# Kernel optimization log

Measured on AMD Instinct MI355X. Metric: run time of the kernel, lower is better.

The kernel has to match this reference:

```python
import jax, jax.numpy as jnp
import numpy as np

N = 100000      # nodes
E = 1250000     # edges
F_IN = 32       # node_feat_dim
H = 64          # hidden_dim (hard-coded in module)
R = 8           # num_relations
G = 256         # graphs in batch
EMB = 16        # embedding_dim
OUT = 1         # output_dim
EPS = 1e-5


def setup_inputs() -> dict:
    key = jax.random.key(0)
    ks = jax.random.split(key, 40)
    w = lambda k, shape: (jax.random.normal(k, shape, jnp.float32) * 0.05)
    inp = {
        'x': jax.random.normal(ks[0], (N, F_IN), jnp.float32),
        'edge_index': jax.random.randint(ks[1], (2, E), 0, N),
        'edge_type': jax.random.randint(ks[2], (E,), 0, R),
        'batch': jnp.sort(jax.random.randint(ks[3], (N,), 0, G)),
        # RGCN layer params: per-relation weight, root weight, bias
        'conv1_w': w(ks[4], (R, F_IN, H)), 'conv1_root': w(ks[5], (F_IN, H)), 'conv1_b': jnp.zeros((H,), jnp.float32),
        'bn1_g': jnp.ones((H,), jnp.float32), 'bn1_b': jnp.zeros((H,), jnp.float32),
        'conv2_w': w(ks[6], (R, H, H)), 'conv2_root': w(ks[7], (H, H)), 'conv2_b': jnp.zeros((H,), jnp.float32),
        'bn2_g': jnp.ones((H,), jnp.float32), 'bn2_b': jnp.zeros((H,), jnp.float32),
        'conv3_w': w(ks[8], (R, H, H)), 'conv3_root': w(ks[9], (H, H)), 'conv3_b': jnp.zeros((H,), jnp.float32),
        'bn3_g': jnp.ones((H,), jnp.float32), 'bn3_b': jnp.zeros((H,), jnp.float32),
        # fc_emb: Linear(384->128), BN(128), LeakyReLU, Dropout(eval=id), Linear(128->EMB)
        'fc1_w': w(ks[10], (3 * H * 2, 128)), 'fc1_b': jnp.zeros((128,), jnp.float32),
        'fcbn_g': jnp.ones((128,), jnp.float32), 'fcbn_b': jnp.zeros((128,), jnp.float32),
        'fc2_w': w(ks[11], (128, EMB)), 'fc2_b': jnp.zeros((EMB,), jnp.float32),
        # decoder: Linear(EMB->64), LeakyReLU, Linear(64->OUT)
        'dec1_w': w(ks[12], (EMB, 64)), 'dec1_b': jnp.zeros((64,), jnp.float32),
        'dec2_w': w(ks[13], (64, OUT)), 'dec2_b': jnp.zeros((OUT,), jnp.float32),
    }
    return inp


def _leaky(z):
    return jnp.where(z > 0, z, 0.2 * z)


def _bn(x, g, b):  # training-mode batch norm, biased variance
    mu = x.mean(axis=0)
    var = x.var(axis=0)
    return g * (x - mu) * jax.lax.rsqrt(var + EPS) + b


def _rgcn(x, W, root, bias, src, dst, edge_type):
    # out_i = x_i @ root + bias + sum_r mean_{j in N_r(i)} x_j @ W_r
    out = x @ root + bias
    for r in range(R):
        mask = (edge_type == r).astype(x.dtype)           # [E]
        h = x @ W[r]                                      # [N, out]
        msg = h[src] * mask[:, None]                      # gather + mask
        s = jax.ops.segment_sum(msg, dst, num_segments=N)  # scatter-add
        cnt = jax.ops.segment_sum(mask, dst, num_segments=N)
        out = out + s / jnp.maximum(cnt, 1.0)[:, None]
    return out


def reference(x, edge_index, edge_type, batch,
              conv1_w, conv1_root, conv1_b, bn1_g, bn1_b,
              conv2_w, conv2_root, conv2_b, bn2_g, bn2_b,
              conv3_w, conv3_root, conv3_b, bn3_g, bn3_b,
              fc1_w, fc1_b, fcbn_g, fcbn_b, fc2_w, fc2_b,
              dec1_w, dec1_b, dec2_w, dec2_b):
    src, dst = edge_index[0], edge_index[1]
    x1 = jax.nn.relu(_bn(_rgcn(x, conv1_w, conv1_root, conv1_b, src, dst, edge_type), bn1_g, bn1_b))
    x2 = jax.nn.relu(_bn(_rgcn(x1, conv2_w, conv2_root, conv2_b, src, dst, edge_type), bn2_g, bn2_b))
    x3 = jax.nn.relu(_bn(_rgcn(x2, conv3_w, conv3_root, conv3_b, src, dst, edge_type), bn3_g, bn3_b))
    x_all = jnp.concatenate([x1, x2, x3], axis=1)         # [N, 3H]
    ones = jnp.ones((N,), x.dtype)
    cnt = jax.ops.segment_sum(ones, batch, num_segments=G)
    pool_mean = jax.ops.segment_sum(x_all, batch, num_segments=G) / jnp.maximum(cnt, 1.0)[:, None]
    pool_max = jax.ops.segment_max(x_all, batch, num_segments=G)
    pool_max = jnp.where(jnp.isfinite(pool_max), pool_max, 0.0)
    x_graph = jnp.concatenate([pool_mean, pool_max], axis=1)  # [G, 6H]
    h = _leaky(_bn(x_graph @ fc1_w + fc1_b, fcbn_g, fcbn_b))  # dropout = identity (eval)
    emb = h @ fc2_w + fc2_b                                   # [G, EMB]
    pred = _leaky(emb @ dec1_w + dec1_b) @ dec2_w + dec2_b    # [G, OUT]
    return (pred, emb)
```

## Files before the change

kernel.cpp:

```cpp
#include <hip/hip_runtime.h>

#define NN 100000
#define NE 1250000
#define FIN 32
#define HD 64
#define NR 8
#define NG 256
#define BN_EPS 1e-5f
#define PCH 100
#define M_KEYS (NN * NR)
#define NB 782
#define RREP 32
#define HW 576

#if defined(__has_builtin)
#if __has_builtin(__builtin_amdgcn_fdot2_f32_bf16)
#define USE_DOT2 1
#endif
#endif
#ifndef USE_DOT2
#define USE_DOT2 0
#endif

typedef unsigned short ushort_t;
typedef __attribute__((ext_vector_type(8))) short short8;
typedef __attribute__((ext_vector_type(4))) float f32x4;
typedef __attribute__((ext_vector_type(4))) unsigned int u32x4;
#if USE_DOT2
typedef __bf16 bf16x2 __attribute__((ext_vector_type(2)));
#endif

static __device__ __forceinline__ ushort_t f2bf(float f) {
  unsigned u = __float_as_uint(f);
  u += 0x7fffu + ((u >> 16) & 1u);
  return (ushort_t)(u >> 16);
}
static __device__ __forceinline__ float bf2f(ushort_t b) {
  return __uint_as_float((unsigned)b << 16);
}

__global__ void k_zero(float* __restrict__ p, int n) {
  int i = blockIdx.x * 256 + threadIdx.x;
  if (i < n) p[i] = 0.0f;
}

__global__ void k_cnt(const int* __restrict__ dst, const int* __restrict__ ty,
                      unsigned* __restrict__ cnt, int* __restrict__ rank) {
  int e = blockIdx.x * 256 + threadIdx.x;
  if (e < NE) {
    int key = dst[e] * NR + ty[e];
    rank[e] = (int)atomicAdd(&cnt[key], 1u);
  }
}

__global__ void k_scanA(const unsigned* __restrict__ cnt, unsigned* __restrict__ bsum) {
  __shared__ unsigned red[256];
  int t = threadIdx.x;
  int base = blockIdx.x * 1024 + t * 4;
  unsigned s = 0;
  #pragma unroll
  for (int i = 0; i < 4; i++) {
    int idx = base + i;
    if (idx < M_KEYS) s += cnt[idx];
  }
  red[t] = s;
  __syncthreads();
  for (int off = 128; off > 0; off >>= 1) {
    if (t < off) red[t] += red[t + off];
    __syncthreads();
  }
  if (t == 0) bsum[blockIdx.x] = red[0];
}

__global__ __launch_bounds__(1024) void k_scanB(const unsigned* __restrict__ bsum,
                                                unsigned* __restrict__ boff,
                                                int* __restrict__ rowstart) {
  __shared__ unsigned sb[1024];
  int t = threadIdx.x;
  unsigned mine = (t < NB) ? bsum[t] : 0u;
  sb[t] = mine;
  __syncthreads();
  for (int off = 1; off < 1024; off <<= 1) {
    unsigned v = (t >= off) ? sb[t - off] : 0u;
    __syncthreads();
    sb[t] += v;
    __syncthreads();
  }
  if (t < NB) boff[t] = sb[t] - mine;
  if (t == 1023) rowstart[M_KEYS] = (int)sb[1023];
}

__global__ void k_scanC(const unsigned* __restrict__ cnt, const unsigned* __restrict__ boff,
                        int* __restrict__ rowstart) {
  __shared__ unsigned sb[256];
  int t = threadIdx.x;
  int base = blockIdx.x * 1024 + t * 4;
  unsigned c0 = (base + 0 < M_KEYS) ? cnt[base + 0] : 0u;
  unsigned c1 = (base + 1 < M_KEYS) ? cnt[base + 1] : 0u;
  unsigned c2 = (base + 2 < M_KEYS) ? cnt[base + 2] : 0u;
  unsigned c3 = (base + 3 < M_KEYS) ? cnt[base + 3] : 0u;
  unsigned tot = c0 + c1 + c2 + c3;
  sb[t] = tot;
  __syncthreads();
  for (int off = 1; off < 256; off <<= 1) {
    unsigned v = (t >= off) ? sb[t - off] : 0u;
    __syncthreads();
    sb[t] += v;
    __syncthreads();
  }
  unsigned run = boff[blockIdx.x] + (sb[t] - tot);
  if (base + 0 < M_KEYS) rowstart[base + 0] = (int)run; run += c0;
  if (base + 1 < M_KEYS) rowstart[base + 1] = (int)run; run += c1;
  if (base + 2 < M_KEYS) rowstart[base + 2] = (int)run; run += c2;
  if (base + 3 < M_KEYS) rowstart[base + 3] = (int)run;
}

__global__ void k_place(const int* __restrict__ src, const int* __restrict__ dst,
                        const int* __restrict__ ty, const int* __restrict__ rank,
                        const int* __restrict__ rowstart, unsigned* __restrict__ eb) {
  int e = blockIdx.x * 256 + threadIdx.x;
  if (e < NE) {
    int t = ty[e];
    int key = dst[e] * NR + t;
    unsigned off = (unsigned)(src[e] * HW + t * 64);
    eb[rowstart[key] + rank[e]] = (off << 3) | (unsigned)t;
  }
}

template <int F>
__global__ void k_wconv(const float* __restrict__ convw, const float* __restrict__ root,
                        ushort_t* __restrict__ wt) {
  int i = blockIdx.x * 256 + threadIdx.x;
  if (i >= 576 * F) return;
  int c = i / F, k = i % F;
  float v = (c < 512) ? convw[((size_t)(c >> 6) * F + k) * 64 + (c & 63)]
                      : root[(size_t)k * 64 + (c & 63)];
  wt[(size_t)c * F + k] = f2bf(v);
}

template <int F, bool APPLY_BN>
__global__ __launch_bounds__(256) void k_xmm(
    const float* __restrict__ xin, const float* __restrict__ scsh,
    const ushort_t* __restrict__ wt, ushort_t* __restrict__ h) {
  constexpr int KK = 2 * F;
  constexpr int XPAD = KK + 8;
  constexpr int LDR = 592;
  __shared__ ushort_t xs[16 * XPAD];
  __shared__ ushort_t ot[16 * LDR];
  int lane = threadIdx.x & 63;
  int w = threadIdx.x >> 6;
  int m = lane & 15;
  int q = lane >> 4;
  int ct0 = w * 9;

  short8 bfrag[9 * (F / 32)];
  #pragma unroll
  for (int ks = 0; ks < F / 32; ks++)
    #pragma unroll
    for (int t = 0; t < 9; t++)
      bfrag[ks * 9 + t] =
          *(const short8*)(wt + (size_t)((ct0 + t) * 16 + m) * F + ks * 32 + q * 8);

  for (int tile = blockIdx.x; tile < NN / 16; tile += gridDim.x) {
    int nbase = tile * 16;
    for (int i = threadIdx.x; i < 16 * F; i += 256) {
      int r = i / F, k = i - r * F;
      float v = xin[(size_t)(nbase + r) * F + k];
      if (APPLY_BN) v = fmaxf(fmaf(v, scsh[k], scsh[64 + k]), 0.0f);
      ushort_t hi = f2bf(v);
      xs[r * XPAD + k] = hi;
      xs[r * XPAD + F + k] = f2bf(v - bf2f(hi));
    }
    __syncthreads();

    short8 afrag[2 * (F / 32)];
    #pragma unroll
    for (int ks = 0; ks < F / 32; ks++) {
      afrag[2 * ks + 0] = *(const short8*)&xs[m * XPAD + ks * 32 + q * 8];
      afrag[2 * ks + 1] = *(const short8*)&xs[m * XPAD + F + ks * 32 + q * 8];
    }

    f32x4 acc[9];
    #pragma unroll
    for (int t = 0; t < 9; t++) acc[t] = (f32x4){0.f, 0.f, 0.f, 0.f};
    #pragma unroll
    for (int ks = 0; ks < F / 32; ks++) {
      #pragma unroll
      for (int t = 0; t < 9; t++) {
        acc[t] = __builtin_amdgcn_mfma_f32_16x16x32_bf16(afrag[2 * ks + 0],
                                                         bfrag[ks * 9 + t], acc[t], 0, 0, 0);
        acc[t] = __builtin_amdgcn_mfma_f32_16x16x32_bf16(afrag[2 * ks + 1],
                                                         bfrag[ks * 9 + t], acc[t], 0, 0, 0);
      }
    }
    #pragma unroll
    for (int t = 0; t < 9; t++) {
      int col = (ct0 + t) * 16 + m;
      #pragma unroll
      for (int j = 0; j < 4; j++) {
        int row = q * 4 + j;
        ot[row * LDR + col] = f2bf(acc[t][j]);
      }
    }
    __syncthreads();
    u32x4* dst = (u32x4*)(h + (size_t)nbase * HW);
    for (int idx = threadIdx.x; idx < 16 * 72; idx += 256) {
      int row = idx / 72, i = idx - row * 72;
      dst[row * 72 + i] = *(const u32x4*)&ot[row * LDR + i * 8];
    }
  }
}

__global__ __launch_bounds__(256) void k_agg4(
    const ushort_t* __restrict__ h, const int* __restrict__ rs,
    const unsigned* __restrict__ eb, const float* __restrict__ bias,
    float* __restrict__ outp, float* __restrict__ statsrep) {
  __shared__ float red[512];
  __shared__ ushort_t iclu[4][8];
  int lane = threadIdx.x & 63, w = threadIdx.x >> 6;
  int n = blockIdx.x * 4 + w;
  if (lane < 8) {
    int c = rs[n * NR + lane + 1] - rs[n * NR + lane];
    iclu[w][lane] = f2bf(1.0f / (float)(c > 1 ? c : 1));
  }
  int lo = rs[n * NR];
  int cnt = rs[n * NR + NR] - lo;
  __syncthreads();
  int g = lane >> 4;
  int c4 = (lane & 15) * 4;
  float a0 = 0.f, a1 = 0.f, a2 = 0.f, a3 = 0.f;
  for (int base = 0; base < cnt; base += 32) {
    unsigned rec[8]; uint2 hv[8]; unsigned icb[8];
    #pragma unroll
    for (int s = 0; s < 8; s++) {
      int el = base + s * 4 + g;
      rec[s] = eb[lo + (el < cnt ? el : cnt - 1)];
      icb[s] = (el < cnt) ? (unsigned)iclu[w][rec[s] & 7] : 0u;
    }
    #pragma unroll
    for (int s = 0; s < 8; s++)
      hv[s] = *(const uint2*)(h + (size_t)(rec[s] >> 3) + c4);
#if USE_DOT2
    #pragma unroll
    for (int s = 0; s < 8; s += 2) {
      unsigned b01 = __builtin_amdgcn_perm(icb[s + 1], icb[s], 0x05040100u);
      unsigned p0 = __builtin_amdgcn_perm(hv[s + 1].x, hv[s].x, 0x05040100u);
      unsigned p1 = __builtin_amdgcn_perm(hv[s + 1].x, hv[s].x, 0x07060302u);
      unsigned p2 = __builtin_amdgcn_perm(hv[s + 1].y, hv[s].y, 0x05040100u);
      unsigned p3 = __builtin_amdgcn_perm(hv[s + 1].y, hv[s].y, 0x07060302u);
      bf16x2 bb = __builtin_bit_cast(bf16x2, b01);
      a0 = __builtin_amdgcn_fdot2_f32_bf16(__builtin_bit_cast(bf16x2, p0), bb, a0, false);
      a1 = __builtin_amdgcn_fdot2_f32_bf16(__builtin_bit_cast(bf16x2, p1), bb, a1, false);
      a2 = __builtin_amdgcn_fdot2_f32_bf16(__builtin_bit_cast(bf16x2, p2), bb, a2, false);
      a3 = __builtin_amdgcn_fdot2_f32_bf16(__builtin_bit_cast(bf16x2, p3), bb, a3, false);
    }
#else
    #pragma unroll
    for (int s = 0; s < 8; s++) {
      float ic = bf2f((ushort_t)icb[s]);
      a0 = fmaf(__uint_as_float(hv[s].x << 16), ic, a0);
      a1 = fmaf(__uint_as_float(hv[s].x & 0xffff0000u), ic, a1);
      a2 = fmaf(__uint_as_float(hv[s].y << 16), ic, a2);
      a3 = fmaf(__uint_as_float(hv[s].y & 0xffff0000u), ic, a3);
    }
#endif
  }
  a0 += __shfl_xor(a0, 16); a0 += __shfl_xor(a0, 32);
  a1 += __shfl_xor(a1, 16); a1 += __shfl_xor(a1, 32);
  a2 += __shfl_xor(a2, 16); a2 += __shfl_xor(a2, 32);
  a3 += __shfl_xor(a3, 16); a3 += __shfl_xor(a3, 32);
  if (g == 0) {
    uint2 sv = *(const uint2*)(h + (size_t)n * HW + 512 + c4);
    float4 b4 = *(const float4*)(bias + c4);
    float d0 = a0 + __uint_as_float(sv.x << 16) + b4.x;
    float d1 = a1 + __uint_as_float(sv.x & 0xffff0000u) + b4.y;
    float d2 = a2 + __uint_as_float(sv.y << 16) + b4.z;
    float d3 = a3 + __uint_as_float(sv.y & 0xffff0000u) + b4.w;
    *(float4*)(outp + (size_t)n * HD + c4) = make_float4(d0, d1, d2, d3);
    *(float4*)(&red[w * 64 + c4]) = make_float4(d0, d1, d2, d3);
    *(float4*)(&red[256 + w * 64 + c4]) =
        make_float4(d0 * d0, d1 * d1, d2 * d2, d3 * d3);
  }
  __syncthreads();
  if (w == 0) {
    float ts = red[lane] + red[64 + lane] + red[128 + lane] + red[192 + lane];
    float tss = red[256 + lane] + red[320 + lane] + red[384 + lane] + red[448 + lane];
    int rp = blockIdx.x & (RREP - 1);
    atomicAdd(&statsrep[rp * 128 + lane], ts);
    atomicAdd(&statsrep[rp * 128 + 64 + lane], tss);
  }
}

__global__ void k_finstats(const float* __restrict__ rep, const float* __restrict__ g,
                           const float* __restrict__ b, float* __restrict__ scsh) {
  int lane = threadIdx.x;
  float s = 0.f, ss = 0.f;
  for (int rp = 0; rp < RREP; rp++) {
    s += rep[rp * 128 + lane];
    ss += rep[rp * 128 + 64 + lane];
  }
  float mu = s * (1.0f / NN);
  float var = ss * (1.0f / NN) - mu * mu;
  float sc = g[lane] * rsqrtf(var + BN_EPS);
  scsh[lane] = sc;
  scsh[64 + lane] = b[lane] - mu * sc;
}

__global__ void k_poolseg(const float* __restrict__ t1, const float* __restrict__ t2,
                          const float* __restrict__ t3, const float* __restrict__ scsh,
                          const int* __restrict__ batch, float* __restrict__ psum,
                          unsigned* __restrict__ pmax, float* __restrict__ cntg) {
  __shared__ int bsh[PCH];
  int base = blockIdx.x * PCH;
  int c = threadIdx.x;
  for (int i = c; i < PCH; i += 192) bsh[i] = batch[base + i];
  __syncthreads();
  int L = c >> 6, cc = c & 63;
  const float* xs = (L == 0) ? t1 : (L == 1) ? t2 : t3;
  float sc = scsh[L * 128 + cc], sh = scsh[L * 128 + 64 + cc];
  int cur = bsh[0];
  float sum = 0.0f, mx = 0.0f;
  int runlen = 0;
  #pragma unroll 4
  for (int i = 0; i < PCH; i++) {
    int g = bsh[i];
    float v = fmaxf(fmaf(xs[(size_t)(base + i) * 64 + cc], sc, sh), 0.0f);
    if (g != cur) {
      atomicAdd(&psum[cur * 192 + c], sum);
      atomicMax(&pmax[cur * 192 + c], __float_as_uint(mx));
      if (c == 0) atomicAdd(&cntg[cur], (float)runlen);
      cur = g; sum = 0.0f; mx = 0.0f; runlen = 0;
    }
    sum += v;
    mx = fmaxf(mx, v);
    runlen++;
  }
  atomicAdd(&psum[cur * 192 + c], sum);
  atomicMax(&pmax[cur * 192 + c], __float_as_uint(mx));
  if (c == 0) atomicAdd(&cntg[cur], (float)runlen);
}

__global__ void k_fc1(const float* __restrict__ psum, const unsigned* __restrict__ pmax,
                      const float* __restrict__ cntg, const float* __restrict__ w,
                      const float* __restrict__ bias, float* __restrict__ h1) {
  __shared__ float a[384];
  int g = blockIdx.x;
  float ic = 1.0f / fmaxf(cntg[g], 1.0f);
  for (int c = threadIdx.x; c < 384; c += 128) {
    a[c] = (c < 192) ? psum[g * 192 + c] * ic : __uint_as_float(pmax[g * 192 + (c - 192)]);
  }
  __syncthreads();
  int j = threadIdx.x;
  float acc = bias[j];
  for (int k = 0; k < 384; k++) acc = fmaf(a[k], w[k * 128 + j], acc);
  h1[g * 128 + j] = acc;
}

__global__ void k_fcbn_stats(const float* __restrict__ h1, const float* __restrict__ g,
                             const float* __restrict__ b, float* __restrict__ scsh) {
  __shared__ float sr[512], ssr[512];
  int j = threadIdx.x & 127, q = threadIdx.x >> 7;
  float s = 0.f, ss = 0.f;
  for (int i = q * 64; i < q * 64 + 64; i++) {
    float v = h1[i * 128 + j];
    s += v;
    ss = fmaf(v, v, ss);
  }
  sr[threadIdx.x] = s;
  ssr[threadIdx.x] = ss;
  __syncthreads();
  if (q == 0) {
    s = sr[j] + sr[128 + j] + sr[256 + j] + sr[384 + j];
    ss = ssr[j] + ssr[128 + j] + ssr[256 + j] + ssr[384 + j];
    float mu = s * (1.0f / NG);
    float var = ss * (1.0f / NG) - mu * mu;
    float sc = g[j] * rsqrtf(var + BN_EPS);
    scsh[j] = sc;
    scsh[128 + j] = b[j] - mu * sc;
  }
}

__global__ void k_leaky(float* __restrict__ h1, const float* __restrict__ scsh) {
  int j = threadIdx.x;
  int g = blockIdx.x;
  float v = fmaf(h1[g * 128 + j], scsh[j], scsh[128 + j]);
  h1[g * 128 + j] = v > 0.0f ? v : 0.2f * v;
}

__global__ void k_head(const float* __restrict__ h1, const float* __restrict__ fc2w,
                       const float* __restrict__ fc2b, const float* __restrict__ d1w,
                       const float* __restrict__ d1b, const float* __restrict__ d2w,
                       const float* __restrict__ d2b, float* __restrict__ out) {
  __shared__ float emb[16];
  int g = blockIdx.x;
  int t = threadIdx.x;
  if (t < 16) {
    float acc = fc2b[t];
    for (int k = 0; k < 128; k++) acc = fmaf(h1[g * 128 + k], fc2w[k * 16 + t], acc);
    emb[t] = acc;
    out[NG + g * 16 + t] = acc;
  }
  __syncthreads();
  float acc = d1b[t];
  for (int k = 0; k < 16; k++) acc = fmaf(emb[k], d1w[k * 64 + t], acc);
  acc = acc > 0.0f ? acc : 0.2f * acc;
  float p = acc * d2w[t];
  for (int off = 32; off > 0; off >>= 1) p += __shfl_down(p, off);
  if (t == 0) out[g] = p + d2b[0];
}

extern "C" void kernel_launch(void* const* d_in, const int* in_sizes, int n_in,
                              void* d_out, int out_size, void* d_ws, size_t ws_size,
                              hipStream_t stream) {
  const float* x    = (const float*)d_in[0];
  const int*   ei   = (const int*)d_in[1];
  const int*   ety  = (const int*)d_in[2];
  const int*   batch= (const int*)d_in[3];
  const float* c1w  = (const float*)d_in[4];
  const float* c1r  = (const float*)d_in[5];
  const float* c1b  = (const float*)d_in[6];
  const float* bn1g = (const float*)d_in[7];
  const float* bn1b = (const float*)d_in[8];
  const float* c2w  = (const float*)d_in[9];
  const float* c2r  = (const float*)d_in[10];
  const float* c2b  = (const float*)d_in[11];
  const float* bn2g = (const float*)d_in[12];
  const float* bn2b = (const float*)d_in[13];
  const float* c3w  = (const float*)d_in[14];
  const float* c3r  = (const float*)d_in[15];
  const float* c3b  = (const float*)d_in[16];
  const float* bn3g = (const float*)d_in[17];
  const float* bn3b = (const float*)d_in[18];
  const float* fc1w = (const float*)d_in[19];
  const float* fc1b = (const float*)d_in[20];
  const float* fbg  = (const float*)d_in[21];
  const float* fbb  = (const float*)d_in[22];
  const float* fc2w = (const float*)d_in[23];
  const float* fc2b = (const float*)d_in[24];
  const float* d1w  = (const float*)d_in[25];
  const float* d1b  = (const float*)d_in[26];
  const float* d2w  = (const float*)d_in[27];
  const float* d2b  = (const float*)d_in[28];
  const int* esrc = ei;
  const int* edst = ei + NE;
  float* out = (float*)d_out;

  float* W = (float*)d_ws;
  size_t o = 0;
  auto alloc = [&](size_t n) { float* p = W + o; o += (n + 63) & ~(size_t)63; return p; };
  unsigned* cnt      = (unsigned*)alloc(M_KEYS);
  float*    psum     = alloc(NG * 192);
  unsigned* pmax     = (unsigned*)alloc(NG * 192);
  float*    cntg     = alloc(NG);
  float*    statsrep = alloc(3 * RREP * 128);
  size_t zone = o;
  int*      rowstart = (int*)alloc(M_KEYS + 1);
  int*      rank = (int*)alloc(NE);
  unsigned* eb   = (unsigned*)alloc(NE);
  unsigned* bsum = (unsigned*)alloc(1024);
  unsigned* boff = (unsigned*)alloc(1024);
  float*    scsh = alloc(3 * 128);
  float*    fcsc = alloc(256);
  float*    h1   = alloc(NG * 128);
  float*    tmp1 = alloc((size_t)NN * HD);
  float*    tmp2 = alloc((size_t)NN * HD);
  float*    tmp3 = alloc((size_t)NN * HD);
  ushort_t* hbig = (ushort_t*)alloc((size_t)NN * HW / 2);
  ushort_t* wt1  = (ushort_t*)alloc(576 * FIN / 2);
  ushort_t* wt2  = (ushort_t*)alloc(576 * HD / 2);
  ushort_t* wt3  = (ushort_t*)alloc(576 * HD / 2);
  (void)ws_size; (void)in_sizes; (void)n_in; (void)out_size;

  k_zero<<<(int)((zone + 255) / 256), 256, 0, stream>>>(W, (int)zone);
  k_cnt<<<(NE + 255) / 256, 256, 0, stream>>>(edst, ety, cnt, rank);
  k_scanA<<<NB, 256, 0, stream>>>(cnt, bsum);
  k_scanB<<<1, 1024, 0, stream>>>(bsum, boff, rowstart);
  k_scanC<<<NB, 256, 0, stream>>>(cnt, boff, rowstart);
  k_place<<<(NE + 255) / 256, 256, 0, stream>>>(esrc, edst, ety, rank, rowstart, eb);
  k_wconv<FIN><<<(576 * FIN + 255) / 256, 256, 0, stream>>>(c1w, c1r, wt1);
  k_wconv<HD><<<(576 * HD + 255) / 256, 256, 0, stream>>>(c2w, c2r, wt2);
  k_wconv<HD><<<(576 * HD + 255) / 256, 256, 0, stream>>>(c3w, c3r, wt3);

  k_xmm<FIN, false><<<1024, 256, 0, stream>>>(x, nullptr, wt1, hbig);
  k_agg4<<<NN / 4, 256, 0, stream>>>(hbig, rowstart, eb, c1b, tmp1, statsrep);
  k_finstats<<<1, 64, 0, stream>>>(statsrep, bn1g, bn1b, scsh);

  k_xmm<HD, true><<<1024, 256, 0, stream>>>(tmp1, scsh, wt2, hbig);
  k_agg4<<<NN / 4, 256, 0, stream>>>(hbig, rowstart, eb, c2b, tmp2, statsrep + RREP * 128);
  k_finstats<<<1, 64, 0, stream>>>(statsrep + RREP * 128, bn2g, bn2b, scsh + 128);

  k_xmm<HD, true><<<1024, 256, 0, stream>>>(tmp2, scsh + 128, wt3, hbig);
  k_agg4<<<NN / 4, 256, 0, stream>>>(hbig, rowstart, eb, c3b, tmp3, statsrep + 2 * RREP * 128);
  k_finstats<<<1, 64, 0, stream>>>(statsrep + 2 * RREP * 128, bn3g, bn3b, scsh + 256);

  k_poolseg<<<NN / PCH, 192, 0, stream>>>(tmp1, tmp2, tmp3, scsh, batch, psum, pmax, cntg);
  k_fc1<<<NG, 128, 0, stream>>>(psum, pmax, cntg, fc1w, fc1b, h1);
  k_fcbn_stats<<<1, 512, 0, stream>>>(h1, fbg, fbb, fcsc);
  k_leaky<<<NG, 128, 0, stream>>>(h1, fcsc);
  k_head<<<NG, 64, 0, stream>>>(h1, fc2w, fc2b, d1w, d1b, d2w, d2b, out);
}
```

Measured before the change: 461.6 us.

## Co-schedule edge counting with layer-1 transform and pooling with later transforms

Merges the edge-count kernel into the layer-1 feature transform launch as extra blocks, and splits the final pooling so each layer's pooling runs as extra blocks inside the next layer's transform kernel. Only the layer-3 pooling is left as a standalone kernel. The aim is to overlap independent work, cutting launch count and idle tail time. The merged kernels share launch bounds and shared-memory allocation across both roles, which can lower occupancy for the lighter branch.

```diff
diff --git a/kernel.cpp b/kernel.cpp
--- a/kernel.cpp
+++ b/kernel.cpp
@@ -12,6 +12,8 @@
 #define NB 782
 #define RREP 32
 #define HW 576
+#define NXB 1024
+#define NCB ((NE + 255) / 256)
 
 #if defined(__has_builtin)
 #if __has_builtin(__builtin_amdgcn_fdot2_f32_bf16)
@@ -42,15 +44,6 @@
 __global__ void k_zero(float* __restrict__ p, int n) {
   int i = blockIdx.x * 256 + threadIdx.x;
   if (i < n) p[i] = 0.0f;
-}
-
-__global__ void k_cnt(const int* __restrict__ dst, const int* __restrict__ ty,
-                      unsigned* __restrict__ cnt, int* __restrict__ rank) {
-  int e = blockIdx.x * 256 + threadIdx.x;
-  if (e < NE) {
-    int key = dst[e] * NR + ty[e];
-    rank[e] = (int)atomicAdd(&cnt[key], 1u);
-  }
 }
 
 __global__ void k_scanA(const unsigned* __restrict__ cnt, unsigned* __restrict__ bsum) {
@@ -139,7 +132,7 @@
 }
 
 template <int F, bool APPLY_BN>
-__global__ __launch_bounds__(256) void k_xmm(
+static __device__ __forceinline__ void xmm_body(
     const float* __restrict__ xin, const float* __restrict__ scsh,
     const ushort_t* __restrict__ wt, ushort_t* __restrict__ h) {
   constexpr int KK = 2 * F;
@@ -161,7 +154,7 @@
       bfrag[ks * 9 + t] =
           *(const short8*)(wt + (size_t)((ct0 + t) * 16 + m) * F + ks * 32 + q * 8);
 
-  for (int tile = blockIdx.x; tile < NN / 16; tile += gridDim.x) {
+  for (int tile = blockIdx.x; tile < NN / 16; tile += NXB) {
     int nbase = tile * 16;
     for (int i = threadIdx.x; i < 16 * F; i += 256) {
       int r = i / F, k = i - r * F;
@@ -209,6 +202,72 @@
       dst[row * 72 + i] = *(const u32x4*)&ot[row * LDR + i * 8];
     }
   }
+}
+
+static __device__ __forceinline__ void pool_body(
+    int pb, const float* __restrict__ t, const float* __restrict__ scshL,
+    const int* __restrict__ batch, float* __restrict__ psum,
+    unsigned* __restrict__ pmax, float* __restrict__ cntg, int poolL, bool addcnt) {
+  __shared__ int bsh[4][PCH];
+  int w = threadIdx.x >> 6, lane = threadIdx.x & 63;
+  int base = (pb * 4 + w) * PCH;
+  for (int i = lane; i < PCH; i += 64) bsh[w][i] = batch[base + i];
+  __syncthreads();
+  float sc = scshL[lane], sh = scshL[64 + lane];
+  int cur = bsh[w][0];
+  float sum = 0.f, mx = 0.f;
+  int runlen = 0;
+  #pragma unroll 4
+  for (int i = 0; i < PCH; i++) {
+    int g = bsh[w][i];
+    float v = fmaxf(fmaf(t[(size_t)(base + i) * 64 + lane], sc, sh), 0.0f);
+    if (g != cur) {
+      atomicAdd(&psum[cur * 192 + poolL * 64 + lane], sum);
+      atomicMax(&pmax[cur * 192 + poolL * 64 + lane], __float_as_uint(mx));
+      if (lane == 0 && addcnt) atomicAdd(&cntg[cur], (float)runlen);
+      cur = g; sum = 0.f; mx = 0.f; runlen = 0;
+    }
+    sum += v;
+    mx = fmaxf(mx, v);
+    runlen++;
+  }
+  atomicAdd(&psum[cur * 192 + poolL * 64 + lane], sum);
+  atomicMax(&pmax[cur * 192 + poolL * 64 + lane], __float_as_uint(mx));
+  if (lane == 0 && addcnt) atomicAdd(&cntg[cur], (float)runlen);
+}
+
+__global__ __launch_bounds__(256) void k_front(
+    const float* __restrict__ x, const ushort_t* __restrict__ wt1,
+    ushort_t* __restrict__ h, const int* __restrict__ dst,
+    const int* __restrict__ ty, unsigned* __restrict__ cnt, int* __restrict__ rank) {
+  if (blockIdx.x < NXB) {
+    xmm_body<FIN, false>(x, nullptr, wt1, h);
+  } else {
+    int e = (blockIdx.x - NXB) * 256 + threadIdx.x;
+    if (e < NE) {
+      int key = dst[e] * NR + ty[e];
+      rank[e] = (int)atomicAdd(&cnt[key], 1u);
+    }
+  }
+}
+
+__global__ __launch_bounds__(256) void k_mid(
+    const float* __restrict__ xin, const float* __restrict__ scsh,
+    const ushort_t* __restrict__ wt, ushort_t* __restrict__ h,
+    const int* __restrict__ batch, float* __restrict__ psum,
+    unsigned* __restrict__ pmax, float* __restrict__ cntg, int poolL) {
+  if (blockIdx.x < NXB) {
+    xmm_body<HD, true>(xin, scsh, wt, h);
+  } else {
+    pool_body(blockIdx.x - NXB, xin, scsh, batch, psum, pmax, cntg, poolL, poolL == 0);
+  }
+}
+
+__global__ __launch_bounds__(256) void k_pool3(
+    const float* __restrict__ t, const float* __restrict__ scshL,
+    const int* __restrict__ batch, float* __restrict__ psum,
+    unsigned* __restrict__ pmax, float* __restrict__ cntg) {
+  pool_body(blockIdx.x, t, scshL, batch, psum, pmax, cntg, 2, false);
 }
 
 __global__ __launch_bounds__(256) void k_agg4(
@@ -304,40 +363,6 @@
   float sc = g[lane] * rsqrtf(var + BN_EPS);
   scsh[lane] = sc;
   scsh[64 + lane] = b[lane] - mu * sc;
-}
-
-__global__ void k_poolseg(const float* __restrict__ t1, const float* __restrict__ t2,
-                          const float* __restrict__ t3, const float* __restrict__ scsh,
-                          const int* __restrict__ batch, float* __restrict__ psum,
-                          unsigned* __restrict__ pmax, float* __restrict__ cntg) {
-  __shared__ int bsh[PCH];
-  int base = blockIdx.x * PCH;
-  int c = threadIdx.x;
-  for (int i = c; i < PCH; i += 192) bsh[i] = batch[base + i];
-  __syncthreads();
-  int L = c >> 6, cc = c & 63;
-  const float* xs = (L == 0) ? t1 : (L == 1) ? t2 : t3;
-  float sc = scsh[L * 128 + cc], sh = scsh[L * 128 + 64 + cc];
-  int cur = bsh[0];
-  float sum = 0.0f, mx = 0.0f;
-  int runlen = 0;
-  #pragma unroll 4
-  for (int i = 0; i < PCH; i++) {
-    int g = bsh[i];
-    float v = fmaxf(fmaf(xs[(size_t)(base + i) * 64 + cc], sc, sh), 0.0f);
-    if (g != cur) {
-      atomicAdd(&psum[cur * 192 + c], sum);
-      atomicMax(&pmax[cur * 192 + c], __float_as_uint(mx));
-      if (c == 0) atomicAdd(&cntg[cur], (float)runlen);
-      cur = g; sum = 0.0f; mx = 0.0f; runlen = 0;
-    }
-    sum += v;
-    mx = fmaxf(mx, v);
-    runlen++;
-  }
-  atomicAdd(&psum[cur * 192 + c], sum);
-  atomicMax(&pmax[cur * 192 + c], __float_as_uint(mx));
-  if (c == 0) atomicAdd(&cntg[cur], (float)runlen);
 }
 
 __global__ void k_fc1(const float* __restrict__ psum, const unsigned* __restrict__ pmax,
@@ -472,28 +497,28 @@
   (void)ws_size; (void)in_sizes; (void)n_in; (void)out_size;
 
   k_zero<<<(int)((zone + 255) / 256), 256, 0, stream>>>(W, (int)zone);
-  k_cnt<<<(NE + 255) / 256, 256, 0, stream>>>(edst, ety, cnt, rank);
+  k_wconv<FIN><<<(576 * FIN + 255) / 256, 256, 0, stream>>>(c1w, c1r, wt1);
+  k_wconv<HD><<<(576 * HD + 255) / 256, 256, 0, stream>>>(c2w, c2r, wt2);
+  k_wconv<HD><<<(576 * HD + 255) / 256, 256, 0, stream>>>(c3w, c3r, wt3);
+
+  k_front<<<NXB + NCB, 256, 0, stream>>>(x, wt1, hbig, edst, ety, cnt, rank);
   k_scanA<<<NB, 256, 0, stream>>>(cnt, bsum);
   k_scanB<<<1, 1024, 0, stream>>>(bsum, boff, rowstart);
   k_scanC<<<NB, 256, 0, stream>>>(cnt, boff, rowstart);
   k_place<<<(NE + 255) / 256, 256, 0, stream>>>(esrc, edst, ety, rank, rowstart, eb);
-  k_wconv<FIN><<<(576 * FIN + 255) / 256, 256, 0, stream>>>(c1w, c1r, wt1);
-  k_wconv<HD><<<(576 * HD + 255) / 256, 256, 0, stream>>>(c2w, c2r, wt2);
-  k_wconv<HD><<<(576 * HD + 255) / 256, 256, 0, stream>>>(c3w, c3r, wt3);
-
-  k_xmm<FIN, false><<<1024, 256, 0, stream>>>(x, nullptr, wt1, hbig);
+
   k_agg4<<<NN / 4, 256, 0, stream>>>(hbig, rowstart, eb, c1b, tmp1, statsrep);
   k_finstats<<<1, 64, 0, stream>>>(statsrep, bn1g, bn1b, scsh);
 
-  k_xmm<HD, true><<<1024, 256, 0, stream>>>(tmp1, scsh, wt2, hbig);
+  k_mid<<<NXB + 250, 256, 0, stream>>>(tmp1, scsh, wt2, hbig, batch, psum, pmax, cntg, 0);
   k_agg4<<<NN / 4, 256, 0, stream>>>(hbig, rowstart, eb, c2b, tmp2, statsrep + RREP * 128);
   k_finstats<<<1, 64, 0, stream>>>(statsrep + RREP * 128, bn2g, bn2b, scsh + 128);
 
-  k_xmm<HD, true><<<1024, 256, 0, stream>>>(tmp2, scsh + 128, wt3, hbig);
+  k_mid<<<NXB + 250, 256, 0, stream>>>(tmp2, scsh + 128, wt3, hbig, batch, psum, pmax, cntg, 1);
   k_agg4<<<NN / 4, 256, 0, stream>>>(hbig, rowstart, eb, c3b, tmp3, statsrep + 2 * RREP * 128);
   k_finstats<<<1, 64, 0, stream>>>(statsrep + 2 * RREP * 128, bn3g, bn3b, scsh + 256);
 
-  k_poolseg<<<NN / PCH, 192, 0, stream>>>(tmp1, tmp2, tmp3, scsh, batch, psum, pmax, cntg);
+  k_pool3<<<250, 256, 0, stream>>>(tmp3, scsh + 256, batch, psum, pmax, cntg);
   k_fc1<<<NG, 128, 0, stream>>>(psum, pmax, cntg, fc1w, fc1b, h1);
   k_fcbn_stats<<<1, 512, 0, stream>>>(h1, fbg, fbb, fcsc);
   k_leaky<<<NG, 128, 0, stream>>>(h1, fcsc);
```

After: 470.3 us. About the same (+1.9%).
